# Kernel tuning notes

Measured on AMD Instinct MI355X. Metric: run time of the kernel, lower is better.

Reference implementation:

```python
import jax, jax.numpy as jnp
import numpy as np

FEAT = 128
BATCH = 4
T_VAL = 256
TAU_VAL = 256
N_NODES = T_VAL + TAU_VAL
NUM_SAMPLES = 5


def _linear_init(key, fan_in, fan_out):
    s = 1.0 / np.sqrt(fan_in)
    kw, kb = jax.random.split(key)
    W = jax.random.uniform(kw, (fan_in, fan_out), minval=-s, maxval=s, dtype=jnp.float32)
    b = jax.random.uniform(kb, (fan_out,), minval=-s, maxval=s, dtype=jnp.float32)
    return W, b


def setup_inputs() -> dict:
    key = jax.random.key(0)
    k0, k1, k2, k3 = jax.random.split(key, 4)
    W1, b1 = _linear_init(k0, 2 * FEAT, FEAT)
    W2, b2 = _linear_init(k1, FEAT, FEAT)
    W3, b3 = _linear_init(k2, FEAT, 1)
    nodes = jax.random.normal(k3, (BATCH, N_NODES, FEAT), dtype=jnp.float32)
    return dict(
        nodes=nodes,
        W1=W1, b1=b1, g1=jnp.ones((FEAT,), jnp.float32), be1=jnp.zeros((FEAT,), jnp.float32),
        W2=W2, b2=b2, g2=jnp.ones((FEAT,), jnp.float32), be2=jnp.zeros((FEAT,), jnp.float32),
        W3=W3, b3=b3,
        T=T_VAL, taus=TAU_VAL, B=BATCH,
    )


def _layernorm(h, g, b):
    mu = h.mean(-1, keepdims=True)
    var = ((h - mu) ** 2).mean(-1, keepdims=True)
    return (h - mu) / jnp.sqrt(var + 1e-5) * g + b


def reference(nodes, W1, b1, g1, be1, W2, b2, g2, be2, W3, b3, T, taus, B):
    N = nodes.shape[1]  # = T + taus
    # Static tril edge structure (uniform T, taus across batch): rows=sink, cols=source
    rows, cols = np.tril_indices(N, -1)
    keep = rows > T  # strictly greater, as in the torch code
    sink_idx = jnp.asarray(rows[keep])   # [E]
    src_idx = jnp.asarray(cols[keep])    # [E]
    E = sink_idx.shape[0]

    # Gather node pairs -> [B, E, 2F]
    net_in = jnp.concatenate([nodes[:, sink_idx], nodes[:, src_idx]], axis=-1)

    # Small MLP: Linear-ReLU-LN x2 + Linear -> logits [B, E]
    h = _layernorm(jax.nn.relu(net_in @ W1 + b1), g1, be1)
    h = _layernorm(jax.nn.relu(h @ W2 + b2), g2, be2)
    logits = (h @ W3 + b3)[..., 0]

    # Gumbel-softmax (hard, tau=1) over edges, NUM_SAMPLES samples per batch
    gkey = jax.random.key(42)
    gnoise = jax.random.gumbel(gkey, (logits.shape[0], NUM_SAMPLES, E), dtype=logits.dtype)
    y_soft = jax.nn.softmax(logits[:, None, :] + gnoise, axis=-1)  # [B, S, E]
    y_hard = jax.nn.one_hot(jnp.argmax(y_soft, axis=-1), E, dtype=y_soft.dtype)
    y = y_hard + y_soft - jax.lax.stop_gradient(y_soft)  # straight-through hard sample

    counts = y.sum(axis=1)  # [B, E], in [0, S]
    # StraightThroughEstimator: forward binarize >0, identity gradient
    path = (counts > 0).astype(counts.dtype) + counts - jax.lax.stop_gradient(counts)

    # Scatter into dense adjacency (dense form of the sparse COO output)
    bidx = jnp.arange(nodes.shape[0])[:, None]
    adj = jnp.zeros((nodes.shape[0], N, N), nodes.dtype)
    adj = adj.at[bidx, sink_idx[None, :], src_idx[None, :]].set(path)
    return adj
```

## Files before the change

kernel.cpp:

```cpp
#include <hip/hip_runtime.h>
#include <stdint.h>

#define FEAT 128
#define NNODES 512
#define BATCH 4
#define EDGES 97920
#define BE (BATCH*EDGES)
#define NSAMP 5
#define BASE_OFF 32896
#define CHUNKS 40
#define NWT (BE/32)
#define MLP_GRID 510
#define MAP_BLOCKS 383

typedef float f32x4 __attribute__((ext_vector_type(4)));
typedef short s16x8 __attribute__((ext_vector_type(8)));

__device__ __forceinline__ void threefry2x32(uint32_t k0, uint32_t k1,
                                             uint32_t& x0, uint32_t& x1) {
  uint32_t k2 = k0 ^ k1 ^ 0x1BD11BDAu;
  x0 += k0; x1 += k1;
#define RR(r) { x0 += x1; x1 = (x1 << (r)) | (x1 >> (32 - (r))); x1 ^= x0; }
  RR(13) RR(15) RR(26) RR(6)   x0 += k1; x1 += k2 + 1u;
  RR(17) RR(29) RR(16) RR(24)  x0 += k2; x1 += k0 + 2u;
  RR(13) RR(15) RR(26) RR(6)   x0 += k0; x1 += k1 + 3u;
  RR(17) RR(29) RR(16) RR(24)  x0 += k1; x1 += k2 + 4u;
  RR(13) RR(15) RR(26) RR(6)   x0 += k2; x1 += k0 + 5u;
#undef RR
}

__device__ __forceinline__ float gumbel_valf(uint32_t n) {
  uint32_t x0 = 0u, x1 = n;
  threefry2x32(0u, 42u, x0, x1);
  uint32_t bits = x0 ^ x1;
  uint32_t fb = (bits >> 9) | 0x3f800000u;
  float f = __uint_as_float(fb) - 1.0f;
  float u = fmaxf(f, 1.1754943508222875e-38f);
  return -logf(-logf(u));
}

__global__ __launch_bounds__(256) void setup_kernel(
    const float* __restrict__ nodes, const float* __restrict__ W1,
    const float* __restrict__ b1, const float* __restrict__ W2,
    const float* __restrict__ g1, const float* __restrict__ be1,
    const float* __restrict__ b2, const float* __restrict__ g2,
    const float* __restrict__ be2, const float* __restrict__ W3,
    const float* __restrict__ b3, float* __restrict__ P, float* __restrict__ Q,
    int2* __restrict__ map, unsigned short* __restrict__ GFH,
    unsigned short* __restrict__ GFL, float* __restrict__ SG,
    float* __restrict__ SB, float* __restrict__ GW3, float* __restrict__ SC) {
  const int blk = blockIdx.x;
  const int tid = threadIdx.x;
  if (blk < 256) {
    __shared__ float snode[8][FEAT];
    const int row0 = blk * 8;
    for (int i = tid; i < 8 * FEAT; i += 256)
      snode[i >> 7][i & 127] = nodes[row0 * FEAT + i];
    __syncthreads();
    const int j = tid & 127;
    const int half = tid >> 7;
    const float* w = W1 + half * FEAT * FEAT + j;
    float acc[8] = {0, 0, 0, 0, 0, 0, 0, 0};
    for (int k = 0; k < FEAT; ++k) {
      float wv = w[k * FEAT];
#pragma unroll
      for (int m = 0; m < 8; ++m) acc[m] += snode[m][k] * wv;
    }
    const float bv = half ? 0.0f : b1[j];
    float* out = half ? Q : P;
#pragma unroll
    for (int m = 0; m < 8; ++m) out[(row0 + m) * FEAT + j] = acc[m] + bv;
  } else if (blk < 256 + MAP_BLOCKS) {
    int e = (blk - 256) * 256 + tid;
    if (e < EDGES) {
      double x = (double)(e + BASE_OFF);
      int s = (int)((1.0 + sqrt(1.0 + 8.0 * x)) * 0.5);
      while ((long long)s * (s - 1) / 2 - BASE_OFF > e) --s;
      while ((long long)(s + 1) * s / 2 - BASE_OFF <= e) ++s;
      int src = e - (int)((long long)s * (s - 1) / 2 - BASE_OFF);
      map[e] = make_int2(s, src);
    }
  } else {
    for (int idx = tid; idx < FEAT * FEAT; idx += 256) {
      const int j = idx & 7;
      const int lane = (idx >> 3) & 63;
      const int nt = (idx >> 9) & 7;
      const int kt = (idx >> 12) & 3;
      const int n = nt * 16 + (lane & 15);
      const int k = kt * 32 + ((lane >> 4) << 3) + j;
      const float g = g1[k] * W2[k * FEAT + n];
      const uint32_t gu = __float_as_uint(g);
      const float d = g - __uint_as_float(gu & 0xFFFF0000u);
      GFH[idx] = (unsigned short)(gu >> 16);
      GFL[idx] = (unsigned short)(__float_as_uint(d) >> 16);
    }
    if (tid < FEAT) {
      float sg = 0.f, sb = 0.f;
      for (int k = 0; k < FEAT; ++k) {
        const float w = W2[k * FEAT + tid];
        sg = fmaf(g1[k], w, sg);
        sb = fmaf(be1[k], w, sb);
      }
      SG[tid] = sg;
      SB[tid] = sb + b2[tid];
      GW3[tid] = g2[tid] * W3[tid];
    }
    __syncthreads();
    if (tid == 0) {
      float a = 0.f, c = 0.f;
      for (int n = 0; n < FEAT; ++n) { a += GW3[n]; c = fmaf(be2[n], W3[n], c); }
      SC[0] = a; SC[1] = c + b3[0];
    }
  }
}

__global__ __launch_bounds__(256, 2) void mlp_kernel(
    const float* __restrict__ P, const float* __restrict__ Q,
    const int2* __restrict__ map,
    const unsigned short* __restrict__ GFH,
    const unsigned short* __restrict__ GFL,
    const float* __restrict__ SG, const float* __restrict__ SB,
    const float* __restrict__ GW3, const float* __restrict__ SC,
    float* __restrict__ logits) {
  __shared__ s16x8 sBH[2048];
  __shared__ s16x8 sBL[2048];
  const int tid = threadIdx.x;
  const int lane = tid & 63;
  const int wave = tid >> 6;
  const int cl = lane & 15;
  const int qd = lane >> 4;

  {
    const float4* s1p = (const float4*)GFH;
    const float4* s2p = (const float4*)GFL;
    float4* d1 = (float4*)sBH;
    float4* d2 = (float4*)sBL;
    for (int i = tid; i < 2048; i += 256) { d1[i] = s1p[i]; d2[i] = s2p[i]; }
  }
  __syncthreads();

  const float sgw3 = SC[0], cb = SC[1];

#pragma unroll 1
  for (int it = 0; it < 6; ++it) {
    const int wt = blockIdx.x * 24 + it * 4 + wave;
    const int g0 = wt * 32;
    const int b = g0 / EDGES;
    const int e0 = g0 - b * EDGES;
    const int bofs = (b << 9);

    s16x8 Ah[2][4], Al[2][4];
    float s1v[2], q1v[2];
#pragma unroll
    for (int mt = 0; mt < 2; ++mt) {
      const int2 ss = map[e0 + mt * 16 + cl];
      const float* pr = P + ((size_t)(bofs + ss.x) << 7) + qd * 8;
      const float* qr = Q + ((size_t)(bofs + ss.y) << 7) + qd * 8;
      float s1 = 0.f, q1 = 0.f;
#pragma unroll
      for (int kt = 0; kt < 4; ++kt) {
        const float4 pa = *(const float4*)(pr + kt * 32);
        const float4 pb = *(const float4*)(pr + kt * 32 + 4);
        const float4 qa = *(const float4*)(qr + kt * 32);
        const float4 qb = *(const float4*)(qr + kt * 32 + 4);
        const float uu[8] = {
            fmaxf(pa.x + qa.x, 0.f), fmaxf(pa.y + qa.y, 0.f),
            fmaxf(pa.z + qa.z, 0.f), fmaxf(pa.w + qa.w, 0.f),
            fmaxf(pb.x + qb.x, 0.f), fmaxf(pb.y + qb.y, 0.f),
            fmaxf(pb.z + qb.z, 0.f), fmaxf(pb.w + qb.w, 0.f)};
#pragma unroll
        for (int j = 0; j < 8; ++j) {
          const float h = uu[j];
          s1 += h;
          q1 = fmaf(h, h, q1);
          const uint32_t xu = __float_as_uint(h);
          const float d = h - __uint_as_float(xu & 0xFFFF0000u);
          Ah[mt][kt][j] = (short)(xu >> 16);
          Al[mt][kt][j] = (short)(__float_as_uint(d) >> 16);
        }
      }
      s1v[mt] = s1;
      q1v[mt] = q1;
      __builtin_amdgcn_sched_barrier(0);
    }

    f32x4 acc[2][8];
#pragma unroll
    for (int mt = 0; mt < 2; ++mt)
#pragma unroll
      for (int nt = 0; nt < 8; ++nt) acc[mt][nt] = (f32x4){0.f, 0.f, 0.f, 0.f};

#pragma unroll
    for (int kt = 0; kt < 4; ++kt) {
#pragma unroll
      for (int np = 0; np < 4; ++np) {
        const int n0 = 2 * np, n1 = 2 * np + 1;
        const s16x8 Bh0 = sBH[(kt * 8 + n0) * 64 + lane];
        const s16x8 Bl0 = sBL[(kt * 8 + n0) * 64 + lane];
        const s16x8 Bh1 = sBH[(kt * 8 + n1) * 64 + lane];
        const s16x8 Bl1 = sBL[(kt * 8 + n1) * 64 + lane];
        acc[0][n0] = __builtin_amdgcn_mfma_f32_16x16x32_bf16(Ah[0][kt], Bh0, acc[0][n0], 0, 0, 0);
        acc[1][n0] = __builtin_amdgcn_mfma_f32_16x16x32_bf16(Ah[1][kt], Bh0, acc[1][n0], 0, 0, 0);
        acc[0][n1] = __builtin_amdgcn_mfma_f32_16x16x32_bf16(Ah[0][kt], Bh1, acc[0][n1], 0, 0, 0);
        acc[1][n1] = __builtin_amdgcn_mfma_f32_16x16x32_bf16(Ah[1][kt], Bh1, acc[1][n1], 0, 0, 0);
        acc[0][n0] = __builtin_amdgcn_mfma_f32_16x16x32_bf16(Al[0][kt], Bh0, acc[0][n0], 0, 0, 0);
        acc[1][n0] = __builtin_amdgcn_mfma_f32_16x16x32_bf16(Al[1][kt], Bh0, acc[1][n0], 0, 0, 0);
        acc[0][n1] = __builtin_amdgcn_mfma_f32_16x16x32_bf16(Al[0][kt], Bh1, acc[0][n1], 0, 0, 0);
        acc[1][n1] = __builtin_amdgcn_mfma_f32_16x16x32_bf16(Al[1][kt], Bh1, acc[1][n1], 0, 0, 0);
        acc[0][n0] = __builtin_amdgcn_mfma_f32_16x16x32_bf16(Ah[0][kt], Bl0, acc[0][n0], 0, 0, 0);
        acc[1][n0] = __builtin_amdgcn_mfma_f32_16x16x32_bf16(Ah[1][kt], Bl0, acc[1][n0], 0, 0, 0);
        acc[0][n1] = __builtin_amdgcn_mfma_f32_16x16x32_bf16(Ah[0][kt], Bl1, acc[0][n1], 0, 0, 0);
        acc[1][n1] = __builtin_amdgcn_mfma_f32_16x16x32_bf16(Ah[1][kt], Bl1, acc[1][n1], 0, 0, 0);
        __builtin_amdgcn_sched_barrier(0);
      }
    }

    float mu[2], rs[2];
#pragma unroll
    for (int mt = 0; mt < 2; ++mt) {
      float s1 = s1v[mt], q1 = q1v[mt];
      s1 += __shfl_xor(s1, 16, 64);
      s1 += __shfl_xor(s1, 32, 64);
      q1 += __shfl_xor(q1, 16, 64);
      q1 += __shfl_xor(q1, 32, 64);
      mu[mt] = s1 * (1.0f / 128.0f);
      const float var = fmaxf(q1 * (1.0f / 128.0f) - mu[mt] * mu[mt], 0.0f);
      rs[mt] = rsqrtf(var + 1e-5f);
    }

    int zz;
    asm volatile("v_mov_b32 %0, 0" : "=v"(zz));
    float SGn[8], SBn[8], GWn[8];
#pragma unroll
    for (int nt = 0; nt < 8; ++nt) {
      const int n = nt * 16 + cl + zz;
      SGn[nt] = SG[n];
      SBn[nt] = SB[n];
      GWn[nt] = GW3[n];
    }
#pragma unroll
    for (int mt = 0; mt < 2; ++mt) {
#pragma unroll
      for (int r = 0; r < 4; ++r) {
        const int me = qd * 4 + r;
        const float mue = __shfl(mu[mt], me, 64);
        const float rse = __shfl(rs[mt], me, 64);
        float s2 = 0.f, q2 = 0.f, t = 0.f;
#pragma unroll
        for (int nt = 0; nt < 8; ++nt) {
          const float Sraw = acc[mt][nt][r];
          const float z = fmaf(rse, fmaf(-mue, SGn[nt], Sraw), SBn[nt]);
          const float h2 = fmaxf(z, 0.f);
          s2 += h2;
          q2 = fmaf(h2, h2, q2);
          t = fmaf(h2, GWn[nt], t);
        }
#pragma unroll
        for (int off = 1; off < 16; off <<= 1) {
          s2 += __shfl_xor(s2, off, 64);
          q2 += __shfl_xor(q2, off, 64);
          t  += __shfl_xor(t,  off, 64);
        }
        if (cl == 0) {
          const float mu2 = s2 * (1.0f / 128.0f);
          const float var2 = fmaxf(q2 * (1.0f / 128.0f) - mu2 * mu2, 0.0f);
          const float rs2 = rsqrtf(var2 + 1e-5f);
          logits[g0 + mt * 16 + me] = rs2 * (t - mu2 * sgw3) + cb;
        }
      }
    }
  }
}

__global__ __launch_bounds__(256) void gumbel_kernel(
    const float* __restrict__ logits, float* __restrict__ bestval,
    int* __restrict__ bestidx) {
  const int bs = blockIdx.x / CHUNKS;
  const int chunk = blockIdx.x % CHUNKS;
  const int b = bs / NSAMP;
  const float* lg = logits + b * EDGES;
  float best = -1e30f; int bi = 0x7fffffff;
  for (int e = chunk * 256 + threadIdx.x; e < EDGES; e += CHUNKS * 256) {
    uint32_t n = (uint32_t)(bs * EDGES + e);
    float val = lg[e] + gumbel_valf(n);
    if (val > best) { best = val; bi = e; }
  }
  __shared__ float sv[256];
  __shared__ int si[256];
  sv[threadIdx.x] = best; si[threadIdx.x] = bi;
  __syncthreads();
  for (int off = 128; off; off >>= 1) {
    if (threadIdx.x < off) {
      float ov = sv[threadIdx.x + off]; int oi = si[threadIdx.x + off];
      if (ov > sv[threadIdx.x] ||
          (ov == sv[threadIdx.x] && oi < si[threadIdx.x])) {
        sv[threadIdx.x] = ov; si[threadIdx.x] = oi;
      }
    }
    __syncthreads();
  }
  if (threadIdx.x == 0) { bestval[blockIdx.x] = sv[0]; bestidx[blockIdx.x] = si[0]; }
}

__global__ __launch_bounds__(64) void select_kernel(
    const float* __restrict__ bestval, const int* __restrict__ bestidx,
    const int2* __restrict__ map, float* __restrict__ adj) {
  const int bs = blockIdx.x;
  const int lane = threadIdx.x;
  float v = -1e30f; int idx = 0x7fffffff;
  if (lane < CHUNKS) { v = bestval[bs * CHUNKS + lane]; idx = bestidx[bs * CHUNKS + lane]; }
#pragma unroll
  for (int off = 32; off; off >>= 1) {
    float ov = __shfl_xor(v, off, 64);
    int oi = __shfl_xor(idx, off, 64);
    if (ov > v || (ov == v && oi < idx)) { v = ov; idx = oi; }
  }
  if (lane == 0) {
    int b = bs / NSAMP;
    int2 ss = map[idx];
    adj[((b * NNODES) + ss.x) * NNODES + ss.y] = 1.0f;
  }
}

extern "C" void kernel_launch(void* const* d_in, const int* in_sizes, int n_in,
                              void* d_out, int out_size, void* d_ws, size_t ws_size,
                              hipStream_t stream) {
  const float* nodes = (const float*)d_in[0];
  const float* W1  = (const float*)d_in[1];
  const float* b1  = (const float*)d_in[2];
  const float* g1  = (const float*)d_in[3];
  const float* be1 = (const float*)d_in[4];
  const float* W2  = (const float*)d_in[5];
  const float* b2  = (const float*)d_in[6];
  const float* g2  = (const float*)d_in[7];
  const float* be2 = (const float*)d_in[8];
  const float* W3  = (const float*)d_in[9];
  const float* b3  = (const float*)d_in[10];
  float* adj = (float*)d_out;

  char* ws = (char*)d_ws;
  float* P       = (float*)(ws);
  float* Q       = (float*)(ws + (1 << 20));
  int2*  map     = (int2*) (ws + (2 << 20));
  float* logits  = (float*)(ws + (3 << 20));
  unsigned short* GFH = (unsigned short*)(ws + (5 << 20));
  unsigned short* GFL = (unsigned short*)(ws + (5 << 20) + 32768);
  float* SG      = (float*)(ws + (5 << 20) + 65536);
  float* SB      = (float*)(ws + (5 << 20) + 66048);
  float* GW3     = (float*)(ws + (5 << 20) + 66560);
  float* SC      = (float*)(ws + (5 << 20) + 67072);
  float* bestval = (float*)(ws + (5 << 20) + 131072);
  int*   bestidx = (int*)  (ws + (5 << 20) + 137472);

  hipMemsetAsync(adj, 0, (size_t)out_size * sizeof(float), stream);
  setup_kernel<<<256 + MAP_BLOCKS + 1, 256, 0, stream>>>(
      nodes, W1, b1, W2, g1, be1, b2, g2, be2, W3, b3,
      P, Q, map, GFH, GFL, SG, SB, GW3, SC);
  mlp_kernel<<<MLP_GRID, 256, 0, stream>>>(P, Q, map, GFH, GFL,
                                           SG, SB, GW3, SC, logits);
  gumbel_kernel<<<20 * CHUNKS, 256, 0, stream>>>(logits, bestval, bestidx);
  select_kernel<<<20, 64, 0, stream>>>(bestval, bestidx, map, adj);
}
```

Before: 172.2 us.

## Fuse Gumbel argmax into MLP epilogue via packed 64-bit atomicMax

Removes the logits buffer and the separate gumbel and select kernels. Each wave now writes its 32 logits to shared memory, adds Gumbel noise for all five samples, and wave-reduces an order-preserving packed (value, inverted index) key. It then commits the key with a 64-bit atomicMax into a per-(batch, sample) slot, and a tiny decode kernel writes the adjacency entries. The MFMA loop is also restructured to double-buffer the B-fragment LDS reads one step ahead. This saves two launches and the logits round-trip but adds global atomics, an extra memset, and more registers.

```diff
diff --git a/kernel.cpp b/kernel.cpp
--- a/kernel.cpp
+++ b/kernel.cpp
@@ -8,7 +8,6 @@
 #define BE (BATCH*EDGES)
 #define NSAMP 5
 #define BASE_OFF 32896
-#define CHUNKS 40
 #define NWT (BE/32)
 #define MLP_GRID 510
 #define MAP_BLOCKS 383
@@ -121,9 +120,10 @@
     const unsigned short* __restrict__ GFL,
     const float* __restrict__ SG, const float* __restrict__ SB,
     const float* __restrict__ GW3, const float* __restrict__ SC,
-    float* __restrict__ logits) {
+    unsigned long long* __restrict__ slots) {
   __shared__ s16x8 sBH[2048];
   __shared__ s16x8 sBL[2048];
+  __shared__ float slog[4][32];
   const int tid = threadIdx.x;
   const int lane = tid & 63;
   const int wave = tid >> 6;
@@ -190,29 +190,33 @@
 #pragma unroll
       for (int nt = 0; nt < 8; ++nt) acc[mt][nt] = (f32x4){0.f, 0.f, 0.f, 0.f};
 
-#pragma unroll
-    for (int kt = 0; kt < 4; ++kt) {
-#pragma unroll
-      for (int np = 0; np < 4; ++np) {
-        const int n0 = 2 * np, n1 = 2 * np + 1;
-        const s16x8 Bh0 = sBH[(kt * 8 + n0) * 64 + lane];
-        const s16x8 Bl0 = sBL[(kt * 8 + n0) * 64 + lane];
-        const s16x8 Bh1 = sBH[(kt * 8 + n1) * 64 + lane];
-        const s16x8 Bl1 = sBL[(kt * 8 + n1) * 64 + lane];
-        acc[0][n0] = __builtin_amdgcn_mfma_f32_16x16x32_bf16(Ah[0][kt], Bh0, acc[0][n0], 0, 0, 0);
-        acc[1][n0] = __builtin_amdgcn_mfma_f32_16x16x32_bf16(Ah[1][kt], Bh0, acc[1][n0], 0, 0, 0);
-        acc[0][n1] = __builtin_amdgcn_mfma_f32_16x16x32_bf16(Ah[0][kt], Bh1, acc[0][n1], 0, 0, 0);
-        acc[1][n1] = __builtin_amdgcn_mfma_f32_16x16x32_bf16(Ah[1][kt], Bh1, acc[1][n1], 0, 0, 0);
-        acc[0][n0] = __builtin_amdgcn_mfma_f32_16x16x32_bf16(Al[0][kt], Bh0, acc[0][n0], 0, 0, 0);
-        acc[1][n0] = __builtin_amdgcn_mfma_f32_16x16x32_bf16(Al[1][kt], Bh0, acc[1][n0], 0, 0, 0);
-        acc[0][n1] = __builtin_amdgcn_mfma_f32_16x16x32_bf16(Al[0][kt], Bh1, acc[0][n1], 0, 0, 0);
-        acc[1][n1] = __builtin_amdgcn_mfma_f32_16x16x32_bf16(Al[1][kt], Bh1, acc[1][n1], 0, 0, 0);
-        acc[0][n0] = __builtin_amdgcn_mfma_f32_16x16x32_bf16(Ah[0][kt], Bl0, acc[0][n0], 0, 0, 0);
-        acc[1][n0] = __builtin_amdgcn_mfma_f32_16x16x32_bf16(Ah[1][kt], Bl0, acc[1][n0], 0, 0, 0);
-        acc[0][n1] = __builtin_amdgcn_mfma_f32_16x16x32_bf16(Ah[0][kt], Bl1, acc[0][n1], 0, 0, 0);
-        acc[1][n1] = __builtin_amdgcn_mfma_f32_16x16x32_bf16(Ah[1][kt], Bl1, acc[1][n1], 0, 0, 0);
-        __builtin_amdgcn_sched_barrier(0);
-      }
+    s16x8 cBh0 = sBH[lane], cBl0 = sBL[lane];
+    s16x8 cBh1 = sBH[64 + lane], cBl1 = sBL[64 + lane];
+#pragma unroll
+    for (int g = 0; g < 16; ++g) {
+      const int kt = g >> 2;
+      const int n0 = (g & 3) * 2, n1 = n0 + 1;
+      s16x8 nBh0, nBl0, nBh1, nBl1;
+      if (g < 15) {
+        const int g2 = g + 1;
+        const int base = ((g2 >> 2) * 8 + (g2 & 3) * 2) * 64 + lane;
+        nBh0 = sBH[base];      nBl0 = sBL[base];
+        nBh1 = sBH[base + 64]; nBl1 = sBL[base + 64];
+      }
+      acc[0][n0] = __builtin_amdgcn_mfma_f32_16x16x32_bf16(Ah[0][kt], cBh0, acc[0][n0], 0, 0, 0);
+      acc[1][n0] = __builtin_amdgcn_mfma_f32_16x16x32_bf16(Ah[1][kt], cBh0, acc[1][n0], 0, 0, 0);
+      acc[0][n1] = __builtin_amdgcn_mfma_f32_16x16x32_bf16(Ah[0][kt], cBh1, acc[0][n1], 0, 0, 0);
+      acc[1][n1] = __builtin_amdgcn_mfma_f32_16x16x32_bf16(Ah[1][kt], cBh1, acc[1][n1], 0, 0, 0);
+      acc[0][n0] = __builtin_amdgcn_mfma_f32_16x16x32_bf16(Al[0][kt], cBh0, acc[0][n0], 0, 0, 0);
+      acc[1][n0] = __builtin_amdgcn_mfma_f32_16x16x32_bf16(Al[1][kt], cBh0, acc[1][n0], 0, 0, 0);
+      acc[0][n1] = __builtin_amdgcn_mfma_f32_16x16x32_bf16(Al[0][kt], cBh1, acc[0][n1], 0, 0, 0);
+      acc[1][n1] = __builtin_amdgcn_mfma_f32_16x16x32_bf16(Al[1][kt], cBh1, acc[1][n1], 0, 0, 0);
+      acc[0][n0] = __builtin_amdgcn_mfma_f32_16x16x32_bf16(Ah[0][kt], cBl0, acc[0][n0], 0, 0, 0);
+      acc[1][n0] = __builtin_amdgcn_mfma_f32_16x16x32_bf16(Ah[1][kt], cBl0, acc[1][n0], 0, 0, 0);
+      acc[0][n1] = __builtin_amdgcn_mfma_f32_16x16x32_bf16(Ah[0][kt], cBl1, acc[0][n1], 0, 0, 0);
+      acc[1][n1] = __builtin_amdgcn_mfma_f32_16x16x32_bf16(Ah[1][kt], cBl1, acc[1][n1], 0, 0, 0);
+      __builtin_amdgcn_sched_barrier(0);
+      if (g < 15) { cBh0 = nBh0; cBl0 = nBl0; cBh1 = nBh1; cBl1 = nBl1; }
     }
 
     float mu[2], rs[2];
@@ -261,63 +265,49 @@
           q2 += __shfl_xor(q2, off, 64);
           t  += __shfl_xor(t,  off, 64);
         }
-        if (cl == 0) {
-          const float mu2 = s2 * (1.0f / 128.0f);
-          const float var2 = fmaxf(q2 * (1.0f / 128.0f) - mu2 * mu2, 0.0f);
-          const float rs2 = rsqrtf(var2 + 1e-5f);
-          logits[g0 + mt * 16 + me] = rs2 * (t - mu2 * sgw3) + cb;
+        const float mu2 = s2 * (1.0f / 128.0f);
+        const float var2 = fmaxf(q2 * (1.0f / 128.0f) - mu2 * mu2, 0.0f);
+        const float rs2 = rsqrtf(var2 + 1e-5f);
+        const float lgv = rs2 * (t - mu2 * sgw3) + cb;
+        if (cl == 0) slog[wave][mt * 16 + me] = lgv;
+      }
+    }
+    __builtin_amdgcn_wave_barrier();
+
+    {
+      const int half = lane >> 5;
+      const int eidx = lane & 31;
+      const float lgv = slog[wave][eidx];
+#pragma unroll
+      for (int i = 0; i < 3; ++i) {
+        const int s = (i < 2) ? (2 * i + half) : 4;
+        const uint32_t n = (uint32_t)((b * NSAMP + s) * EDGES + (e0 + eidx));
+        const float val = lgv + gumbel_valf(n);
+        uint32_t u = __float_as_uint(val);
+        u = (u & 0x80000000u) ? ~u : (u | 0x80000000u);
+        unsigned long long pk =
+            ((unsigned long long)u << 32) | (uint32_t)(~(uint32_t)(e0 + eidx));
+#pragma unroll
+        for (int off = 1; off < 32; off <<= 1) {
+          const unsigned long long o = __shfl_xor(pk, off, 64);
+          if (o > pk) pk = o;
         }
-      }
-    }
+        if (eidx == 0) atomicMax(&slots[b * NSAMP + s], pk);
+      }
+    }
+    __builtin_amdgcn_wave_barrier();
   }
 }
 
-__global__ __launch_bounds__(256) void gumbel_kernel(
-    const float* __restrict__ logits, float* __restrict__ bestval,
-    int* __restrict__ bestidx) {
-  const int bs = blockIdx.x / CHUNKS;
-  const int chunk = blockIdx.x % CHUNKS;
-  const int b = bs / NSAMP;
-  const float* lg = logits + b * EDGES;
-  float best = -1e30f; int bi = 0x7fffffff;
-  for (int e = chunk * 256 + threadIdx.x; e < EDGES; e += CHUNKS * 256) {
-    uint32_t n = (uint32_t)(bs * EDGES + e);
-    float val = lg[e] + gumbel_valf(n);
-    if (val > best) { best = val; bi = e; }
-  }
-  __shared__ float sv[256];
-  __shared__ int si[256];
-  sv[threadIdx.x] = best; si[threadIdx.x] = bi;
-  __syncthreads();
-  for (int off = 128; off; off >>= 1) {
-    if (threadIdx.x < off) {
-      float ov = sv[threadIdx.x + off]; int oi = si[threadIdx.x + off];
-      if (ov > sv[threadIdx.x] ||
-          (ov == sv[threadIdx.x] && oi < si[threadIdx.x])) {
-        sv[threadIdx.x] = ov; si[threadIdx.x] = oi;
-      }
-    }
-    __syncthreads();
-  }
-  if (threadIdx.x == 0) { bestval[blockIdx.x] = sv[0]; bestidx[blockIdx.x] = si[0]; }
-}
-
-__global__ __launch_bounds__(64) void select_kernel(
-    const float* __restrict__ bestval, const int* __restrict__ bestidx,
+__global__ __launch_bounds__(64) void decode_kernel(
+    const unsigned long long* __restrict__ slots,
     const int2* __restrict__ map, float* __restrict__ adj) {
-  const int bs = blockIdx.x;
-  const int lane = threadIdx.x;
-  float v = -1e30f; int idx = 0x7fffffff;
-  if (lane < CHUNKS) { v = bestval[bs * CHUNKS + lane]; idx = bestidx[bs * CHUNKS + lane]; }
-#pragma unroll
-  for (int off = 32; off; off >>= 1) {
-    float ov = __shfl_xor(v, off, 64);
-    int oi = __shfl_xor(idx, off, 64);
-    if (ov > v || (ov == v && oi < idx)) { v = ov; idx = oi; }
-  }
-  if (lane == 0) {
-    int b = bs / NSAMP;
-    int2 ss = map[idx];
+  const int l = threadIdx.x;
+  if (l < BATCH * NSAMP) {
+    const unsigned long long pk = slots[l];
+    const int e = (int)(~(uint32_t)(pk & 0xFFFFFFFFu));
+    const int b = l / NSAMP;
+    const int2 ss = map[e];
     adj[((b * NNODES) + ss.x) * NNODES + ss.y] = 1.0f;
   }
 }
@@ -342,22 +332,20 @@
   float* P       = (float*)(ws);
   float* Q       = (float*)(ws + (1 << 20));
   int2*  map     = (int2*) (ws + (2 << 20));
-  float* logits  = (float*)(ws + (3 << 20));
   unsigned short* GFH = (unsigned short*)(ws + (5 << 20));
   unsigned short* GFL = (unsigned short*)(ws + (5 << 20) + 32768);
   float* SG      = (float*)(ws + (5 << 20) + 65536);
   float* SB      = (float*)(ws + (5 << 20) + 66048);
   float* GW3     = (float*)(ws + (5 << 20) + 66560);
   float* SC      = (float*)(ws + (5 << 20) + 67072);
-  float* bestval = (float*)(ws + (5 << 20) + 131072);
-  int*   bestidx = (int*)  (ws + (5 << 20) + 137472);
+  unsigned long long* slots = (unsigned long long*)(ws + (5 << 20) + 131072);
 
   hipMemsetAsync(adj, 0, (size_t)out_size * sizeof(float), stream);
+  hipMemsetAsync(slots, 0, BATCH * NSAMP * sizeof(unsigned long long), stream);
   setup_kernel<<<256 + MAP_BLOCKS + 1, 256, 0, stream>>>(
       nodes, W1, b1, W2, g1, be1, b2, g2, be2, W3, b3,
       P, Q, map, GFH, GFL, SG, SB, GW3, SC);
   mlp_kernel<<<MLP_GRID, 256, 0, stream>>>(P, Q, map, GFH, GFL,
-                                           SG, SB, GW3, SC, logits);
-  gumbel_kernel<<<20 * CHUNKS, 256, 0, stream>>>(logits, bestval, bestidx);
-  select_kernel<<<20, 64, 0, stream>>>(bestval, bestidx, map, adj);
-}
+                                           SG, SB, GW3, SC, slots);
+  decode_kernel<<<1, 64, 0, stream>>>(slots, map, adj);
+}
```

Measured after the change: 438.6 us. 155% more time.
